# Kernel optimization log

Hardware: AMD Instinct MI355X
Metric: run time of the kernel (lower is better)

## Reference

```python
import jax, jax.numpy as jnp
import numpy as np

# PtConv dims from SegSmall: pl=64 channels, n_centers=16 kernel elements, dim=3
B, N, K = 4, 16384, 16          # batch, points, neighbors
C_IN, C_OUT, KS, DIM = 64, 64, 16, 3


def setup_inputs() -> dict:
    key = jax.random.key(0)
    ks = jax.random.split(key, 10)
    features = jax.random.normal(ks[0], (B, N, C_IN), dtype=jnp.float32)
    input_pts = jax.random.uniform(ks[1], (B, N, DIM), dtype=jnp.float32)
    output_pts = input_pts  # same-resolution conv: queries == input points
    indices = jax.random.randint(ks[2], (B, N, K), 0, N)  # precomputed KNN indices
    # weight init as in PtConv
    bound = float(np.sqrt(3.0) * np.sqrt(2.0 / (C_IN + C_OUT)))
    weight = jax.random.uniform(ks[3], (C_IN, KS, C_OUT), jnp.float32, -bound, bound)
    bias = jnp.zeros((C_OUT,), jnp.float32)
    centers = jax.random.uniform(ks[4], (DIM, KS), jnp.float32, -1.0, 1.0)
    # position-MLP params: Linear(dim*KS -> 2*KS), Linear(2*KS -> KS), Linear(KS -> KS)
    def lin(k, fan_in, fan_out):
        lim = 1.0 / np.sqrt(fan_in)
        kw, kb = jax.random.split(k)
        W = jax.random.uniform(kw, (fan_in, fan_out), jnp.float32, -lim, lim)
        b = jax.random.uniform(kb, (fan_out,), jnp.float32, -lim, lim)
        return W, b
    w1, b1 = lin(ks[5], DIM * KS, 2 * KS)
    w2, b2 = lin(ks[6], 2 * KS, KS)
    w3, b3 = lin(ks[7], KS, KS)
    return {"features": features, "input_pts": input_pts, "output_pts": output_pts,
            "weight": weight, "bias": bias, "centers": centers,
            "w1": w1, "b1": b1, "w2": w2, "b2": b2, "w3": w3, "b3": b3,
            "indices": indices}


def reference(features, input_pts, output_pts, weight, bias, centers,
              w1, b1, w2, b2, w3, b3, indices):
    # per-batch gather of neighbor features and coordinates
    gather = jax.vmap(lambda a, idx: a[idx])
    feat_g = gather(features, indices)          # [B, M, K, C_in]
    pts_g = gather(input_pts, indices)          # [B, M, K, 3]
    pts = pts_g - output_pts[:, :, None, :]      # nn_center=True
    # distances to kernel centers: [B,M,K,3,1] - [3,KS] -> [B,M,K,3,KS] -> [B,M,K,3*KS]
    d = (pts[..., None] - centers).reshape(pts.shape[0], pts.shape[1], pts.shape[2], -1)
    d = jax.nn.relu(d @ w1 + b1)
    d = jax.nn.relu(d @ w2 + b2)
    d = jax.nn.relu(d @ w3 + b3)                 # [B, M, K, KS]
    # weighted neighbor aggregation: bmm(features^T, dists)
    agg = jnp.einsum('bmkc,bmkj->bmcj', feat_g, d)   # [B, M, C_in, KS]
    out = jnp.einsum('bmcj,cjo->bmo', agg, weight)   # flatten (C_in,KS) matches weight.view(-1,out)
    out = out / feat_g.shape[2]                      # divide by K (fs[2])
    out = out + bias
    return out
```

## Files before the change

kernel.cpp:

```cpp
#include <hip/hip_runtime.h>

#define NPTS 16384
#define KN   16
#define CIN  64
#define COUT 64
#define KSIZ 16
#define PTS  32

typedef _Float16 h4v    __attribute__((ext_vector_type(4)));
typedef _Float16 h8v    __attribute__((ext_vector_type(8)));
typedef __fp16   fp16x2 __attribute__((ext_vector_type(2)));
typedef float    f32x4  __attribute__((ext_vector_type(4)));

union H2U { fp16x2 h; unsigned u; };
union H4U { h4v v; fp16x2 p[2]; uint2 u2; };
union H8U { h8v v; uint4 u4; };

#define WS_WF_OFF   512
#define WS_F16_OFF  131584
#define WS_NEEDED   (131584ull + 8388608ull)

__global__ void prep_kernel(const float* __restrict__ weight,
                            const float* __restrict__ w1,
                            const float* __restrict__ b1,
                            const float* __restrict__ centers,
                            const float* __restrict__ features,
                            unsigned* __restrict__ wsp,
                            uint4* __restrict__ wf,
                            uint4* __restrict__ fb16) {
    const int b = blockIdx.x;
    const int t = threadIdx.x;
    if (b < 32) {
        const int bp = b*4 + (t>>6);
        const int kk = bp >> 2, nt = bp & 3;
        const int l = t & 63, li = l & 15, g = l >> 4;
        unsigned short u[8];
        #pragma unroll
        for (int e = 0; e < 8; ++e) {
            int s = kk*32 + g*8 + e;
            int j = s >> 6;
            int c = s & 63;
            union { _Float16 h; unsigned short s16; } cv;
            cv.h = (_Float16)(weight[(c*16 + j)*64 + nt*16 + li] * 0.0625f);
            u[e] = cv.s16;
        }
        uint4 v;
        v.x = u[0] | ((unsigned)u[1] << 16);
        v.y = u[2] | ((unsigned)u[3] << 16);
        v.z = u[4] | ((unsigned)u[5] << 16);
        v.w = u[6] | ((unsigned)u[7] << 16);
        wf[(kk*4 + nt)*64 + l] = v;
    } else if (b == 32) {
        __shared__ float tmp[4][32];
        if (t < 32) {
            int n = t;
            float s0 = 0.f, s1 = 0.f, s2 = 0.f, bf = b1[n];
            for (int s = 0; s < KSIZ; ++s) {
                float a0 = w1[(0*KSIZ + s)*32 + n];
                float a1 = w1[(1*KSIZ + s)*32 + n];
                float a2 = w1[(2*KSIZ + s)*32 + n];
                s0 += a0; s1 += a1; s2 += a2;
                bf -= centers[0*KSIZ+s]*a0 + centers[1*KSIZ+s]*a1 + centers[2*KSIZ+s]*a2;
            }
            tmp[0][n] = s0; tmp[1][n] = s1; tmp[2][n] = s2; tmp[3][n] = bf;
        }
        __syncthreads();
        if (t < 64) {
            const int row = t >> 4, q = t & 15;
            union { _Float16 h[2]; unsigned u; } pk;
            pk.h[0] = (_Float16)tmp[row][2*q];
            pk.h[1] = (_Float16)tmp[row][2*q+1];
            wsp[row*16 + q] = pk.u;
        }
    } else {
        const size_t e0 = ((size_t)(b - 33)*256 + t) * 8;
        const float4 f0 = *(const float4*)(features + e0);
        const float4 f1 = *(const float4*)(features + e0 + 4);
        union { _Float16 h[8]; uint4 v; } o;
        o.h[0] = (_Float16)f0.x; o.h[1] = (_Float16)f0.y;
        o.h[2] = (_Float16)f0.z; o.h[3] = (_Float16)f0.w;
        o.h[4] = (_Float16)f1.x; o.h[5] = (_Float16)f1.y;
        o.h[6] = (_Float16)f1.z; o.h[7] = (_Float16)f1.w;
        fb16[e0 >> 3] = o.v;
    }
}

template<int FM>
__global__ __launch_bounds__(512, 4)
void ptconv_kernel(const float* __restrict__ features,
                   const float* __restrict__ input_pts,
                   const float* __restrict__ output_pts,
                   const float* __restrict__ bias,
                   const float* __restrict__ w2,
                   const float* __restrict__ b2,
                   const float* __restrict__ w3,
                   const float* __restrict__ b3,
                   const int*   __restrict__ indices,
                   const unsigned* __restrict__ folded,
                   const uint4* __restrict__ wf,
                   const uint2* __restrict__ fb16,
                   float* __restrict__ out) {
    __shared__ __align__(16) char smem[65536];
    char* s_agg = smem;

    const int t    = threadIdx.x;
    const int l    = t & 63;
    const int wave = t >> 6;
    const int li   = l & 15;
    const int g    = l >> 4;
    const int h    = wave >> 2;
    const int nq   = wave & 3;
    const int m0   = blockIdx.x * PTS;
    const int bbk  = m0 >> 14;
    const int mloc = m0 & (NPTS-1);

    const int*   idxB  = indices    + (size_t)bbk*NPTS*KN;
    const float* ptsB  = input_pts  + (size_t)bbk*NPTS*3;
    const float* optsB = output_pts + (size_t)bbk*NPTS*3;
    const float* fb    = features + (size_t)bbk*NPTS*CIN;
    const uint2* fb16B = fb16 + (size_t)bbk*NPTS*(CIN/4);

    const int p1 = t >> 4, k1 = t & 15;
    const int nn = mloc + p1;
    const int idxv = idxB[nn*KN + k1];
    const float cop0 = optsB[nn*3+0], cop1 = optsB[nn*3+1], cop2 = optsB[nn*3+2];
    const float cip0 = ptsB[(size_t)idxv*3+0];
    const float cip1 = ptsB[(size_t)idxv*3+1];
    const float cip2 = ptsB[(size_t)idxv*3+2];

    const int4 idA = *(const int4*)(idxB + (mloc + wave*4+0)*KN + 4*g);
    const int4 idB = *(const int4*)(idxB + (mloc + wave*4+1)*KN + 4*g);
    const int4 idC = *(const int4*)(idxB + (mloc + wave*4+2)*KN + 4*g);
    const int4 idD = *(const int4*)(idxB + (mloc + wave*4+3)*KN + 4*g);

    H4U gA0, gA1, gA2, gA3, gB0, gB1, gB2, gB3;
    H4U gC0, gC1, gC2, gC3, gD0, gD1, gD2, gD3;
    f32x4 fA0, fA1, fA2, fA3, fB0, fB1, fB2, fB3;
    if constexpr (FM == 1) {
        gA0.u2 = fb16B[(size_t)idA.x*16 + li]; gA1.u2 = fb16B[(size_t)idA.y*16 + li];
        gA2.u2 = fb16B[(size_t)idA.z*16 + li]; gA3.u2 = fb16B[(size_t)idA.w*16 + li];
        gB0.u2 = fb16B[(size_t)idB.x*16 + li]; gB1.u2 = fb16B[(size_t)idB.y*16 + li];
        gB2.u2 = fb16B[(size_t)idB.z*16 + li]; gB3.u2 = fb16B[(size_t)idB.w*16 + li];
        gC0.u2 = fb16B[(size_t)idC.x*16 + li]; gC1.u2 = fb16B[(size_t)idC.y*16 + li];
        gC2.u2 = fb16B[(size_t)idC.z*16 + li]; gC3.u2 = fb16B[(size_t)idC.w*16 + li];
        gD0.u2 = fb16B[(size_t)idD.x*16 + li]; gD1.u2 = fb16B[(size_t)idD.y*16 + li];
        gD2.u2 = fb16B[(size_t)idD.z*16 + li]; gD3.u2 = fb16B[(size_t)idD.w*16 + li];
    } else {
        fA0 = *(const f32x4*)(fb + (size_t)idA.x*CIN + 4*li);
        fA1 = *(const f32x4*)(fb + (size_t)idA.y*CIN + 4*li);
        fA2 = *(const f32x4*)(fb + (size_t)idA.z*CIN + 4*li);
        fA3 = *(const f32x4*)(fb + (size_t)idA.w*CIN + 4*li);
        fB0 = *(const f32x4*)(fb + (size_t)idB.x*CIN + 4*li);
        fB1 = *(const f32x4*)(fb + (size_t)idB.y*CIN + 4*li);
        fB2 = *(const f32x4*)(fb + (size_t)idB.z*CIN + 4*li);
        fB3 = *(const f32x4*)(fb + (size_t)idB.w*CIN + 4*li);
    }

    h8v w2f; h4v w3f;
    #pragma unroll
    for (int e = 0; e < 8; ++e) w2f[e] = (_Float16)w2[(8*g+e)*16 + li];
    #pragma unroll
    for (int e = 0; e < 4; ++e) w3f[e] = (_Float16)w3[(4*g+e)*16 + li];
    const f32x4 b2v4  = *(const f32x4*)(b2 + 4*g);
    const float b3v   = b3[li];
    const float biasO = bias[nq*16 + li];
    const uint4* wp   = wf + nq*64 + l;

    {
        const __fp16 r0h = (__fp16)(cip0-cop0);
        const __fp16 r1h = (__fp16)(cip1-cop1);
        const __fp16 r2h = (__fp16)(cip2-cop2);
        fp16x2 r0p = {r0h, r0h}, r1p = {r1h, r1h}, r2p = {r2h, r2h};
        const fp16x2 zz = {(__fp16)0.f, (__fp16)0.f};
        uint4* dst = (uint4*)(smem + wave*8192 + l*80);
        unsigned o8[8];
        #pragma unroll
        for (int half = 0; half < 2; ++half) {
            #pragma unroll
            for (int qq = 0; qq < 8; ++qq) {
                const int q = half*8 + qq;
                H2U a, u0, u1, u2;
                a.u  = folded[48+q];
                u0.u = folded[q];
                u1.u = folded[16+q];
                u2.u = folded[32+q];
                fp16x2 acc = r0p*u0.h + a.h;
                acc = r1p*u1.h + acc;
                acc = r2p*u2.h + acc;
                acc = __builtin_elementwise_max(acc, zz);
                H2U o; o.h = acc; o8[qq] = o.u;
            }
            dst[half*2+0] = make_uint4(o8[0], o8[1], o8[2], o8[3]);
            dst[half*2+1] = make_uint4(o8[4], o8[5], o8[6], o8[7]);
        }
    }

    h4v dreg0, dreg1, dreg2, dreg3;
#define L23(PP, DREG) { \
    h8v B2 = *(const h8v*)(smem + wave*8192 + ((PP)*16 + li)*80 + g*16); \
    f32x4 a2 = b2v4; \
    a2 = __builtin_amdgcn_mfma_f32_16x16x32_f16(w2f, B2, a2, 0, 0, 0); \
    H4U A3; \
    A3.p[0] = __builtin_amdgcn_cvt_pkrtz(fmaxf(a2[0],0.f), fmaxf(a2[1],0.f)); \
    A3.p[1] = __builtin_amdgcn_cvt_pkrtz(fmaxf(a2[2],0.f), fmaxf(a2[3],0.f)); \
    f32x4 a3 = {b3v, b3v, b3v, b3v}; \
    a3 = __builtin_amdgcn_mfma_f32_16x16x16f16(A3.v, w3f, a3, 0, 0, 0); \
    H4U Dv; \
    Dv.p[0] = __builtin_amdgcn_cvt_pkrtz(fmaxf(a3[0],0.f), fmaxf(a3[1],0.f)); \
    Dv.p[1] = __builtin_amdgcn_cvt_pkrtz(fmaxf(a3[2],0.f), fmaxf(a3[3],0.f)); \
    DREG = Dv.v; }
    L23(0, dreg0) L23(1, dreg1) L23(2, dreg2) L23(3, dreg3)
#undef L23

#define P2STORE(PP, E0,E1,E2,E3) { \
    const int pix_ = wave*4 + (PP); \
    const unsigned swz_ = (unsigned)((pix_ & 7) << 4); \
    char* ab_ = s_agg + pix_*2048; \
    _Pragma("unroll") \
    for (int r = 0; r < 4; ++r) { \
        H2U d01, d23; \
        d01.h = __builtin_amdgcn_cvt_pkrtz(E0[r], E1[r]); \
        d23.h = __builtin_amdgcn_cvt_pkrtz(E2[r], E3[r]); \
        *(uint2*)(ab_ + ((unsigned)((4*g + r)*128 + 8*li) ^ swz_)) = \
            make_uint2(d01.u, d23.u); \
    } }

    if constexpr (FM == 1) {
#define P2F16(PP, R0,R1,R2,R3) { \
        f32x4 z = {0.f,0.f,0.f,0.f}; \
        f32x4 e0_, e1_, e2_, e3_; \
        { H4U B_; B_.v = (h4v){R0.v[0], R1.v[0], R2.v[0], R3.v[0]}; \
          e0_ = __builtin_amdgcn_mfma_f32_16x16x16f16(dreg##PP, B_.v, z, 0, 0, 0); } \
        { H4U B_; B_.v = (h4v){R0.v[1], R1.v[1], R2.v[1], R3.v[1]}; \
          e1_ = __builtin_amdgcn_mfma_f32_16x16x16f16(dreg##PP, B_.v, z, 0, 0, 0); } \
        { H4U B_; B_.v = (h4v){R0.v[2], R1.v[2], R2.v[2], R3.v[2]}; \
          e2_ = __builtin_amdgcn_mfma_f32_16x16x16f16(dreg##PP, B_.v, z, 0, 0, 0); } \
        { H4U B_; B_.v = (h4v){R0.v[3], R1.v[3], R2.v[3], R3.v[3]}; \
          e3_ = __builtin_amdgcn_mfma_f32_16x16x16f16(dreg##PP, B_.v, z, 0, 0, 0); } \
        P2STORE(PP, e0_, e1_, e2_, e3_) }
        P2F16(0, gA0, gA1, gA2, gA3)
        P2F16(1, gB0, gB1, gB2, gB3)
        P2F16(2, gC0, gC1, gC2, gC3)
        P2F16(3, gD0, gD1, gD2, gD3)
#undef P2F16
    } else {
#define P2F32(PP, R0,R1,R2,R3) { \
        f32x4 z = {0.f,0.f,0.f,0.f}; \
        f32x4 e0_, e1_, e2_, e3_; \
        { H4U B_; B_.p[0] = __builtin_amdgcn_cvt_pkrtz(R0[0], R1[0]); \
          B_.p[1] = __builtin_amdgcn_cvt_pkrtz(R2[0], R3[0]); \
          e0_ = __builtin_amdgcn_mfma_f32_16x16x16f16(dreg##PP, B_.v, z, 0, 0, 0); } \
        { H4U B_; B_.p[0] = __builtin_amdgcn_cvt_pkrtz(R0[1], R1[1]); \
          B_.p[1] = __builtin_amdgcn_cvt_pkrtz(R2[1], R3[1]); \
          e1_ = __builtin_amdgcn_mfma_f32_16x16x16f16(dreg##PP, B_.v, z, 0, 0, 0); } \
        { H4U B_; B_.p[0] = __builtin_amdgcn_cvt_pkrtz(R0[2], R1[2]); \
          B_.p[1] = __builtin_amdgcn_cvt_pkrtz(R2[2], R3[2]); \
          e2_ = __builtin_amdgcn_mfma_f32_16x16x16f16(dreg##PP, B_.v, z, 0, 0, 0); } \
        { H4U B_; B_.p[0] = __builtin_amdgcn_cvt_pkrtz(R0[3], R1[3]); \
          B_.p[1] = __builtin_amdgcn_cvt_pkrtz(R2[3], R3[3]); \
          e3_ = __builtin_amdgcn_mfma_f32_16x16x16f16(dreg##PP, B_.v, z, 0, 0, 0); } \
        P2STORE(PP, e0_, e1_, e2_, e3_) }
        P2F32(0, fA0, fA1, fA2, fA3)
        P2F32(1, fB0, fB1, fB2, fB3)
        fA0 = *(const f32x4*)(fb + (size_t)idC.x*CIN + 4*li);
        fA1 = *(const f32x4*)(fb + (size_t)idC.y*CIN + 4*li);
        fA2 = *(const f32x4*)(fb + (size_t)idC.z*CIN + 4*li);
        fA3 = *(const f32x4*)(fb + (size_t)idC.w*CIN + 4*li);
        fB0 = *(const f32x4*)(fb + (size_t)idD.x*CIN + 4*li);
        fB1 = *(const f32x4*)(fb + (size_t)idD.y*CIN + 4*li);
        fB2 = *(const f32x4*)(fb + (size_t)idD.z*CIN + 4*li);
        fB3 = *(const f32x4*)(fb + (size_t)idD.w*CIN + 4*li);
        P2F32(2, fA0, fA1, fA2, fA3)
        P2F32(3, fB0, fB1, fB2, fB3)
#undef P2F32
    }
#undef P2STORE

    uint4 q0 = wp[0*256], q1 = wp[1*256], q2 = wp[2*256], q3 = wp[3*256];
    uint4 q4 = wp[4*256], q5 = wp[5*256], q6 = wp[6*256], q7 = wp[7*256];

    asm volatile("s_waitcnt lgkmcnt(0)" ::: "memory");
    __builtin_amdgcn_s_barrier();
    asm volatile("" ::: "memory");

    __builtin_amdgcn_s_setprio(1);
    f32x4 a0 = {0.f,0.f,0.f,0.f}, a1 = a0, a2 = a0, a3 = a0;
    const unsigned swr = (unsigned)((li & 7) << 4);
#define AREAD(KK) (*(const h8v*)(s_agg + (h*16 + li)*2048 + (((KK)*64 + g*16) ^ swr)))
#define MFS(KK, Q, ACC)  { H8U bu_; bu_.u4 = Q; \
    ACC = __builtin_amdgcn_mfma_f32_16x16x32_f16(AREAD(KK), bu_.v, ACC, 0, 0, 0); }
#define MFSL(KK, Q, ACC) MFS(KK, Q, ACC) Q = wp[((KK)+8)*256];
    MFSL(0, q0, a0) MFSL(1, q1, a1) MFSL(2, q2, a2) MFSL(3, q3, a3)
    MFSL(4, q4, a0) MFSL(5, q5, a1) MFSL(6, q6, a2) MFSL(7, q7, a3)
    MFSL(8, q0, a0) MFSL(9, q1, a1) MFSL(10, q2, a2) MFSL(11, q3, a3)
    MFSL(12, q4, a0) MFSL(13, q5, a1) MFSL(14, q6, a2) MFSL(15, q7, a3)
    MFSL(16, q0, a0) MFSL(17, q1, a1) MFSL(18, q2, a2) MFSL(19, q3, a3)
    MFSL(20, q4, a0) MFSL(21, q5, a1) MFSL(22, q6, a2) MFSL(23, q7, a3)
    MFS(24, q0, a0) MFS(25, q1, a1) MFS(26, q2, a2) MFS(27, q3, a3)
    MFS(28, q4, a0) MFS(29, q5, a1) MFS(30, q6, a2) MFS(31, q7, a3)
#undef MFSL
#undef MFS
#undef AREAD
    __builtin_amdgcn_s_setprio(0);

    const f32x4 acc = (a0 + a1) + (a2 + a3);
    #pragma unroll
    for (int r = 0; r < 4; ++r) {
        const int mr = h*16 + g*4 + r;
        out[(size_t)(m0 + mr)*COUT + nq*16 + li] = acc[r] + biasO;
    }
}

extern "C" void kernel_launch(void* const* d_in, const int* in_sizes, int n_in,
                              void* d_out, int out_size, void* d_ws, size_t ws_size,
                              hipStream_t stream) {
    const float* features   = (const float*)d_in[0];
    const float* input_pts  = (const float*)d_in[1];
    const float* output_pts = (const float*)d_in[2];
    const float* weight     = (const float*)d_in[3];
    const float* bias       = (const float*)d_in[4];
    const float* centers    = (const float*)d_in[5];
    const float* w1         = (const float*)d_in[6];
    const float* b1         = (const float*)d_in[7];
    const float* w2         = (const float*)d_in[8];
    const float* b2         = (const float*)d_in[9];
    const float* w3         = (const float*)d_in[10];
    const float* b3         = (const float*)d_in[11];
    const int*   indices    = (const int*)d_in[12];
    float* out = (float*)d_out;
    unsigned* wsp = (unsigned*)d_ws;
    uint4* wf   = (uint4*)((char*)d_ws + WS_WF_OFF);
    uint4* fb16 = (uint4*)((char*)d_ws + WS_F16_OFF);

    const bool f16ok = ws_size >= WS_NEEDED;
    const int nconv = f16ok ? (4*NPTS*CIN) / (256*8) : 0;
    prep_kernel<<<33 + nconv, 256, 0, stream>>>(
        weight, w1, b1, centers, features, wsp, wf, fb16);

    const int total_pts = 4 * NPTS;
    if (f16ok) {
        ptconv_kernel<1><<<total_pts / PTS, 512, 0, stream>>>(
            features, input_pts, output_pts, bias,
            w2, b2, w3, b3, indices, wsp, wf, (const uint2*)fb16, out);
    } else {
        ptconv_kernel<0><<<total_pts / PTS, 512, 0, stream>>>(
            features, input_pts, output_pts, bias,
            w2, b2, w3, b3, indices, wsp, wf, (const uint2*)fb16, out);
    }
}
```

Baseline: 50.25 us.

## Split GEMM K dimension across wave halves and reduce partials through LDS

Changes the final aggregation GEMM so each wave covers both 16-row point halves but only half of the K range. Each weight B-fragment loaded from global memory then feeds two MFMAs, which halves per-wave weight traffic. The partial sums are combined through shared memory, at the cost of two extra barriers and an LDS round trip. The weight prefetch is also moved earlier to overlap with the gathers, and the coordinate loads are merged into float3 loads.

Result: faster. 42.62 us (-15.2%).

```diff
diff --git a/kernel.cpp b/kernel.cpp
--- a/kernel.cpp
+++ b/kernel.cpp
@@ -108,8 +108,8 @@
     const int wave = t >> 6;
     const int li   = l & 15;
     const int g    = l >> 4;
-    const int h    = wave >> 2;
     const int nq   = wave & 3;
+    const int kkh  = wave >> 2;
     const int m0   = blockIdx.x * PTS;
     const int bbk  = m0 >> 14;
     const int mloc = m0 & (NPTS-1);
@@ -123,10 +123,8 @@
     const int p1 = t >> 4, k1 = t & 15;
     const int nn = mloc + p1;
     const int idxv = idxB[nn*KN + k1];
-    const float cop0 = optsB[nn*3+0], cop1 = optsB[nn*3+1], cop2 = optsB[nn*3+2];
-    const float cip0 = ptsB[(size_t)idxv*3+0];
-    const float cip1 = ptsB[(size_t)idxv*3+1];
-    const float cip2 = ptsB[(size_t)idxv*3+2];
+    const float3 opv = *(const float3*)(optsB + nn*3);
+    const float3 ipv = *(const float3*)(ptsB + (size_t)idxv*3);
 
     const int4 idA = *(const int4*)(idxB + (mloc + wave*4+0)*KN + 4*g);
     const int4 idB = *(const int4*)(idxB + (mloc + wave*4+1)*KN + 4*g);
@@ -156,6 +154,12 @@
         fB3 = *(const f32x4*)(fb + (size_t)idB.w*CIN + 4*li);
     }
 
+    const uint4* wp = wf + nq*64 + l;
+    uint4 q0 = wp[(kkh*16+0)*256], q1 = wp[(kkh*16+1)*256];
+    uint4 q2 = wp[(kkh*16+2)*256], q3 = wp[(kkh*16+3)*256];
+    uint4 q4 = wp[(kkh*16+4)*256], q5 = wp[(kkh*16+5)*256];
+    uint4 q6 = wp[(kkh*16+6)*256], q7 = wp[(kkh*16+7)*256];
+
     h8v w2f; h4v w3f;
     #pragma unroll
     for (int e = 0; e < 8; ++e) w2f[e] = (_Float16)w2[(8*g+e)*16 + li];
@@ -164,12 +168,11 @@
     const f32x4 b2v4  = *(const f32x4*)(b2 + 4*g);
     const float b3v   = b3[li];
     const float biasO = bias[nq*16 + li];
-    const uint4* wp   = wf + nq*64 + l;
 
     {
-        const __fp16 r0h = (__fp16)(cip0-cop0);
-        const __fp16 r1h = (__fp16)(cip1-cop1);
-        const __fp16 r2h = (__fp16)(cip2-cop2);
+        const __fp16 r0h = (__fp16)(ipv.x - opv.x);
+        const __fp16 r1h = (__fp16)(ipv.y - opv.y);
+        const __fp16 r2h = (__fp16)(ipv.z - opv.z);
         fp16x2 r0p = {r0h, r0h}, r1p = {r1h, r1h}, r2p = {r2h, r2h};
         const fp16x2 zz = {(__fp16)0.f, (__fp16)0.f};
         uint4* dst = (uint4*)(smem + wave*8192 + l*80);
@@ -276,38 +279,53 @@
     }
 #undef P2STORE
 
-    uint4 q0 = wp[0*256], q1 = wp[1*256], q2 = wp[2*256], q3 = wp[3*256];
-    uint4 q4 = wp[4*256], q5 = wp[5*256], q6 = wp[6*256], q7 = wp[7*256];
-
     asm volatile("s_waitcnt lgkmcnt(0)" ::: "memory");
     __builtin_amdgcn_s_barrier();
     asm volatile("" ::: "memory");
 
     __builtin_amdgcn_s_setprio(1);
-    f32x4 a0 = {0.f,0.f,0.f,0.f}, a1 = a0, a2 = a0, a3 = a0;
+    f32x4 h0a = {0.f,0.f,0.f,0.f}, h0b = h0a, h1a = h0a, h1b = h0a;
     const unsigned swr = (unsigned)((li & 7) << 4);
-#define AREAD(KK) (*(const h8v*)(s_agg + (h*16 + li)*2048 + (((KK)*64 + g*16) ^ swr)))
-#define MFS(KK, Q, ACC)  { H8U bu_; bu_.u4 = Q; \
-    ACC = __builtin_amdgcn_mfma_f32_16x16x32_f16(AREAD(KK), bu_.v, ACC, 0, 0, 0); }
-#define MFSL(KK, Q, ACC) MFS(KK, Q, ACC) Q = wp[((KK)+8)*256];
-    MFSL(0, q0, a0) MFSL(1, q1, a1) MFSL(2, q2, a2) MFSL(3, q3, a3)
-    MFSL(4, q4, a0) MFSL(5, q5, a1) MFSL(6, q6, a2) MFSL(7, q7, a3)
-    MFSL(8, q0, a0) MFSL(9, q1, a1) MFSL(10, q2, a2) MFSL(11, q3, a3)
-    MFSL(12, q4, a0) MFSL(13, q5, a1) MFSL(14, q6, a2) MFSL(15, q7, a3)
-    MFSL(16, q0, a0) MFSL(17, q1, a1) MFSL(18, q2, a2) MFSL(19, q3, a3)
-    MFSL(20, q4, a0) MFSL(21, q5, a1) MFSL(22, q6, a2) MFSL(23, q7, a3)
-    MFS(24, q0, a0) MFS(25, q1, a1) MFS(26, q2, a2) MFS(27, q3, a3)
-    MFS(28, q4, a0) MFS(29, q5, a1) MFS(30, q6, a2) MFS(31, q7, a3)
-#undef MFSL
-#undef MFS
-#undef AREAD
+#define AR(H, KK) (*(const h8v*)(s_agg + ((H)*16 + li)*2048 + ((((KK))*64 + g*16) ^ swr)))
+#define STEP(S, Q, A0, A1) { H8U bu_; bu_.u4 = Q; \
+    A0 = __builtin_amdgcn_mfma_f32_16x16x32_f16(AR(0, kkh*16+(S)), bu_.v, A0, 0, 0, 0); \
+    A1 = __builtin_amdgcn_mfma_f32_16x16x32_f16(AR(1, kkh*16+(S)), bu_.v, A1, 0, 0, 0); }
+#define STEPL(S, Q, A0, A1) STEP(S, Q, A0, A1) Q = wp[(kkh*16+(S)+8)*256];
+    STEPL(0, q0, h0a, h1a) STEPL(1, q1, h0b, h1b)
+    STEPL(2, q2, h0a, h1a) STEPL(3, q3, h0b, h1b)
+    STEPL(4, q4, h0a, h1a) STEPL(5, q5, h0b, h1b)
+    STEPL(6, q6, h0a, h1a) STEPL(7, q7, h0b, h1b)
+    STEP( 8, q0, h0a, h1a) STEP( 9, q1, h0b, h1b)
+    STEP(10, q2, h0a, h1a) STEP(11, q3, h0b, h1b)
+    STEP(12, q4, h0a, h1a) STEP(13, q5, h0b, h1b)
+    STEP(14, q6, h0a, h1a) STEP(15, q7, h0b, h1b)
+#undef STEPL
+#undef STEP
+#undef AR
     __builtin_amdgcn_s_setprio(0);
-
-    const f32x4 acc = (a0 + a1) + (a2 + a3);
-    #pragma unroll
-    for (int r = 0; r < 4; ++r) {
-        const int mr = h*16 + g*4 + r;
-        out[(size_t)(m0 + mr)*COUT + nq*16 + li] = acc[r] + biasO;
+    f32x4 acc0 = h0a + h0b;
+    f32x4 acc1 = h1a + h1b;
+
+    asm volatile("s_waitcnt lgkmcnt(0)" ::: "memory");
+    __builtin_amdgcn_s_barrier();
+    asm volatile("" ::: "memory");
+    if (wave >= 4) {
+        *(f32x4*)(smem + ((wave-4)*2 + 0)*1024 + l*16) = acc0;
+        *(f32x4*)(smem + ((wave-4)*2 + 1)*1024 + l*16) = acc1;
+    }
+    asm volatile("s_waitcnt lgkmcnt(0)" ::: "memory");
+    __builtin_amdgcn_s_barrier();
+    asm volatile("" ::: "memory");
+    if (wave < 4) {
+        const f32x4 p0 = *(const f32x4*)(smem + (wave*2 + 0)*1024 + l*16);
+        const f32x4 p1 = *(const f32x4*)(smem + (wave*2 + 1)*1024 + l*16);
+        acc0 += p0;
+        acc1 += p1;
+        #pragma unroll
+        for (int r = 0; r < 4; ++r) {
+            out[(size_t)(m0 +      g*4 + r)*COUT + nq*16 + li] = acc0[r] + biasO;
+            out[(size_t)(m0 + 16 + g*4 + r)*COUT + nq*16 + li] = acc1[r] + biasO;
+        }
     }
 }
 
```
